# Performance work log

Measured on AMD Instinct MI355X. Metric: run time of the kernel, lower is better.

The kernel has to match this reference:

```python
import jax, jax.numpy as jnp
import numpy as np

B, M, F_IN, DX, K, L, N_ALL = 8192, 10, 128, 128, 64, 32, 100000
NN = M - 1          # n_neigh
INF = float(M)


def layer_norm(x, g, b, eps=1e-5):
    mu = x.mean(-1, keepdims=True)
    var = ((x - mu) ** 2).mean(-1, keepdims=True)
    return (x - mu) * jax.lax.rsqrt(var + eps) * g + b


def bfs_dists(adj, mask):
    # normalized all-pairs hop distances via repeated boolean matmul (m=10 fixed)
    adj_bin = (adj > 1e-5).astype(jnp.float32)
    eye = jnp.eye(M, dtype=bool)
    d = jnp.where(eye[None], 0.0, jnp.where(adj_bin > 0, 1.0, INF))
    curr = adj_bin
    for k in range(2, M):
        curr = jnp.matmul(curr, adj_bin)
        d = jnp.where((curr > 0) & (d == INF), float(k), d)
    mask2 = mask[:, :, None] * mask[:, None, :]
    d = jnp.where(mask2 == 0, INF, d)
    return d / float(M)


def compute_sw(zb, zp, theta, vmask):
    # sliced Wasserstein-2 between batch point clouds [B,NN,d] and prototypes [K,NN,d]
    tn = theta / jnp.linalg.norm(theta, axis=1, keepdims=True)
    pb = jnp.einsum('bmd,ld->bml', zb, tn)
    pp = jnp.einsum('kmd,ld->kml', zp, tn)
    idx = jnp.argsort(pb, axis=1)
    pbs = jnp.take_along_axis(pb, idx, axis=1)
    pps = jnp.sort(pp, axis=1)
    w = jnp.take_along_axis(jnp.broadcast_to(vmask[:, :, None], pb.shape), idx, axis=1)
    w = w / (w.sum(axis=1, keepdims=True) + 1e-9)
    # sum_m w*(pb-pp)^2 expanded to avoid materializing [B,K,NN,L]
    t1 = (w * pbs ** 2).sum(axis=1)                   # [B,L]
    t2 = jnp.einsum('bml,kml->bkl', w * pbs, pps)     # [B,K,L]
    t3 = jnp.einsum('bml,kml->bkl', w, pps ** 2)
    return (t1[:, None, :] - 2.0 * t2 + t3).mean(axis=-1)


def compute_radial(rb, rp, vmask):
    idx = jnp.argsort(rb, axis=1)
    rbs = jnp.take_along_axis(rb, idx, axis=1)
    rps = jnp.sort(rp, axis=1)
    w = jnp.take_along_axis(vmask, idx, axis=1)
    w = w / (w.sum(axis=1, keepdims=True) + 1e-9)
    return (((rbs[:, None, :] - rps[None]) ** 2) * w[:, None, :]).sum(-1)


def setup_inputs() -> dict:
    key = jax.random.key(0)
    ks = jax.random.split(key, 16)
    up = (jax.random.uniform(ks[0], (B, M, M)) < 0.3).astype(jnp.float32)
    adj = jnp.maximum(up, up.transpose(0, 2, 1)) * (1.0 - jnp.eye(M))
    features = jax.random.normal(ks[1], (N_ALL, F_IN), jnp.float32)
    idxs = jax.random.randint(ks[2], (B, M), 0, N_ALL + 1)   # N_ALL == padding index
    rn = lambda k, s, sc=0.02: sc * jax.random.normal(k, s, jnp.float32)
    params = dict(
        x_lin_w=rn(ks[3], (F_IN, DX), 0.05), x_lin_b=jnp.zeros((DX,)),
        x_ln_g=jnp.ones((DX,)), x_ln_b=jnp.zeros((DX,)),
        s_ln_g=jnp.ones((NN,)), s_ln_b=jnp.zeros((NN,)),
        theta_x=jax.random.normal(ks[4], (L, DX), jnp.float32),
        theta_s=jax.random.normal(ks[5], (L, NN), jnp.float32),
        alpha_raw=jnp.zeros(()),
        an_w1=rn(ks[6], (DX, 32), 0.1), an_b1=jnp.zeros((32,)),
        an_w2=rn(ks[7], (32, 1), 0.1), an_b2=jnp.zeros((1,)),
        wn_w1=rn(ks[8], (2 * DX, 32), 0.1), wn_b1=jnp.zeros((32,)),
        wn_w2=rn(ks[9], (32, 1), 0.1), wn_b2=jnp.zeros((1,)),
        w_raw=jnp.zeros(()),
        proto_root=jax.random.normal(ks[10], (K, F_IN), jnp.float32),
        proto_neigh=jax.random.normal(ks[11], (K, NN, F_IN), jnp.float32),
        proto_rad=jax.random.uniform(ks[12], (K, NN)),
        proto_dn=jax.random.uniform(ks[13], (NN * (NN - 1) // 2, K), minval=-0.5, maxval=0.5),
        log_gamma=jnp.asarray(np.log(0.01), jnp.float32),
    )
    return {"adj": adj, "features": features, "idxs": idxs, **params}


def reference(adj, features, idxs, x_lin_w, x_lin_b, x_ln_g, x_ln_b, s_ln_g, s_ln_b,
              theta_x, theta_s, alpha_raw, an_w1, an_b1, an_w2, an_b2,
              wn_w1, wn_b1, wn_w2, wn_b2, w_raw,
              proto_root, proto_neigh, proto_rad, proto_dn, log_gamma):
    b = adj.shape[0]
    x_all = jnp.concatenate([features, jnp.zeros((1, F_IN), features.dtype)], 0)
    x_patch = x_all[idxs]                             # [B,M,F]
    x_root, x_neigh = x_patch[:, 0], x_patch[:, 1:]
    vmask = (idxs[:, 1:] != N_ALL).astype(jnp.float32)   # [B,NN]
    lin = lambda x: x @ x_lin_w + x_lin_b
    h_root = layer_norm(lin(x_root), x_ln_g, x_ln_b)
    h_proto_root = layer_norm(lin(proto_root), x_ln_g, x_ln_b)
    d_root_feat = (jnp.sum(h_root ** 2, -1)[:, None] + jnp.sum(h_proto_root ** 2, -1)[None]
                   - 2.0 * h_root @ h_proto_root.T)   # squared cdist [B,K]
    full_mask = jnp.concatenate([jnp.ones((b, 1), jnp.float32), vmask], 1)
    dists_full = bfs_dists(adj, full_mask)
    d_radial_str = compute_radial(dists_full[:, 0, 1:], proto_rad, vmask)
    h_neigh = layer_norm(lin(x_neigh), x_ln_g, x_ln_b)     # dropout = identity (eval)
    h_proto_neigh = layer_norm(lin(proto_neigh), x_ln_g, x_ln_b)
    sw_neigh_feat = compute_sw(h_neigh, h_proto_neigh, theta_x, vmask)
    hs_neigh = layer_norm(jnp.sort(dists_full[:, 1:, 1:], axis=1), s_ln_g, s_ln_b)
    ti, tj = np.triu_indices(NN, 1)
    C = jnp.zeros((K, NN, NN)).at[:, ti, tj].set(jax.nn.sigmoid(proto_dn).T)
    C = C + C.transpose(0, 2, 1)
    hs_proto = layer_norm(jnp.sort(C, axis=1), s_ln_g, s_ln_b)
    sw_neigh_str = compute_sw(hs_neigh, hs_proto, theta_s, vmask)
    h_pooled = (h_neigh * vmask[:, :, None]).sum(1) / (vmask.sum(1, keepdims=True) + 1e-9)
    alpha_logit = jnp.maximum(h_pooled @ an_w1 + an_b1, 0.0) @ an_w2 + an_b2   # [B,1]
    alpha = jax.nn.sigmoid(alpha_raw + alpha_logit)
    # pairwise w_net([h_root; h_proto_root]) without materializing [B,K,2*DX]
    hb = h_root @ wn_w1[:DX] + wn_b1                   # [B,32]
    hp = h_proto_root @ wn_w1[DX:]                     # [K,32]
    w_logit = (jnp.maximum(hb[:, None] + hp[None], 0.0) @ wn_w2)[..., 0] + wn_b2[0]
    w = jax.nn.sigmoid(w_raw + w_logit)                # [B,K]
    d_feat = w * d_root_feat + (1.0 - w) * sw_neigh_feat
    d_str = w * d_radial_str + (1.0 - w) * sw_neigh_str
    d_fgw = alpha * d_feat + (1.0 - alpha) * d_str
    return jnp.exp(-jnp.exp(log_gamma) * d_fgw)        # [B,K]
```

## Files before the change

### kernel.cpp

```cpp
#include <hip/hip_runtime.h>
#include <hip/hip_bf16.h>

typedef unsigned short u16;
typedef __attribute__((ext_vector_type(8))) short short8;
typedef __attribute__((ext_vector_type(4))) float f32x4;

#define NN 9
#define DX 128
#define KP 64
#define LL 32
#define NALL 100000
#define BMAX 8192
#define NBM 16
#define NBP 64

#define MFMA(a, b, c) __builtin_amdgcn_mfma_f32_16x16x32_bf16(a, b, c, 0, 0, 0)
#define WFENCE() __threadfence_block()

__device__ __align__(16) float g_tns[LL * NN];
__device__ __align__(16) float g_hprn[KP];
__device__ __align__(16) float g_hpt[32 * KP];
__device__ __align__(16) float g_rpst[NN * KP];
__device__ __align__(16) u16   g_hx[BMAX * 10 * DX];
__device__ __align__(16) u16   g_pW[16384];
__device__ __align__(16) u16   g_pBt[4096];
__device__ __align__(16) u16   g_pBr[8192];
__device__ __align__(16) u16   g_pBx[36864];
__device__ __align__(16) u16   g_pBs[36864];
__device__ __align__(16) u16   g_pAn[4096];
__device__ __align__(16) u16   g_pWn[4096];

__device__ __forceinline__ float bf2f(u16 u) {
    union { unsigned u; float f; } v; v.u = ((unsigned)u) << 16; return v.f;
}
__device__ __forceinline__ u16 f2bf(float f) {
    __hip_bfloat16 h = __float2bfloat16(f);
    union { __hip_bfloat16 h; u16 u; } v; v.h = h; return v.u;
}
__device__ __forceinline__ float ldv(const void* p, long i, int f32) {
    return f32 ? ((const float*)p)[i] : bf2f(((const u16*)p)[i]);
}
__device__ __forceinline__ float sigmoidf(float x) { return 1.f / (1.f + expf(-x)); }

__device__ __forceinline__ int bfrag_idx(int ksteps, int ncol, int kd) {
    int ntile = ncol >> 4, n = ncol & 15;
    int kstep = kd >> 5, quad = (kd >> 3) & 3, j = kd & 7;
    return ((ntile * ksteps + kstep) * 64 + quad * 16 + n) * 8 + j;
}

__device__ __forceinline__ void rank9(const float* v, int* r) {
#pragma unroll
    for (int m = 0; m < 9; m++) {
        int rk = 0;
#pragma unroll
        for (int n = 0; n < 9; n++)
            rk += (v[n] < v[m]) || (v[n] == v[m] && n < m);
        r[m] = rk;
    }
}

__global__ __launch_bounds__(256) void k_pack(
    const void* xlw, const void* theta_x, const void* theta_s,
    const void* an_w1, const void* wn_w1, const void* xlg) {
    int t = threadIdx.x;
    const int f32 = (((const u16*)xlg)[0] == 0);
    if (blockIdx.x == 0) {
        for (int i = t; i < 16384; i += 256) {
            int c = i >> 7, d = i & 127;
            g_pW[bfrag_idx(4, d, c)] = f2bf(ldv(xlw, i, f32));
        }
    } else if (blockIdx.x == 1) {
        if (t < 32) {
            float s = 0;
            for (int d = 0; d < 128; d++) { float v = ldv(theta_x, t * 128 + d, f32); s = fmaf(v, v, s); }
            float inv = 1.f / sqrtf(s);
            for (int d = 0; d < 128; d++)
                g_pBt[bfrag_idx(4, t, d)] = f2bf(ldv(theta_x, t * 128 + d, f32) * inv);
        } else if (t < 64) {
            int l = t - 32;
            float s = 0;
            for (int j = 0; j < 9; j++) { float v = ldv(theta_s, l * 9 + j, f32); s = fmaf(v, v, s); }
            float inv = 1.f / sqrtf(s);
            for (int j = 0; j < 9; j++) g_tns[l * 9 + j] = ldv(theta_s, l * 9 + j, f32) * inv;
        }
    } else {
        for (int i = t; i < 4096; i += 256) {
            int d = i >> 5, j = i & 31;
            g_pAn[bfrag_idx(4, j, d)] = f2bf(ldv(an_w1, i, f32));
            g_pWn[bfrag_idx(4, j, d)] = f2bf(ldv(wn_w1, i, f32));
        }
    }
}

__global__ __launch_bounds__(256, 4) void k_lin(
    const void* feat, const int* idxs,
    const void* proto_root, const void* proto_neigh,
    const void* xlb, const void* xlg, const void* xlbt,
    const void* slg, const void* slb, const void* wn_w1,
    const void* proto_rad, const void* proto_dn, int B) {
    __shared__ __align__(16) u16   WfL[16384];
    __shared__ __align__(16) u16   hXpb[1280];
    __shared__ __align__(16) float pbX[288];
    __shared__ __align__(16) float Cm[84];
    __shared__ __align__(16) float hsnP[84];

    int t = threadIdx.x, lane = t & 63, w = t >> 6;
    const int f32 = (((const u16*)xlg)[0] == 0);
    int fm = lane & 15, quad = lane >> 4;
    bool isProto = (blockIdx.x < (unsigned)NBP);
    int rcap = isProto ? 10 : 60;
    int base = isProto ? blockIdx.x * 10 : (blockIdx.x - NBP) * 60;
    int rowT = isProto ? KP * 10 : B * 10;

    {
        const short8* src = (const short8*)g_pW;
        short8* dst = (short8*)WfL;
#pragma unroll
        for (int i = 0; i < 8; i++) dst[t + 256 * i] = src[t + 256 * i];
    }

    int lr = w * 16 + fm, gr = base + lr;
    bool azero = true;
    const void* abuf = feat; long aoff = 0;
    if (lr < rcap && gr < rowT) {
        if (!isProto) {
            int id = idxs[gr];
            if (id != NALL) { azero = false; aoff = (long)id * 128; }
        } else {
            int rr = gr % 10; azero = false;
            if (rr < 9) { abuf = proto_neigh; aoff = (long)((gr / 10) * 9 + rr) * 128; }
            else        { abuf = proto_root;  aoff = (long)(gr / 10) * 128; }
        }
    }
    short8 af[4];
#pragma unroll
    for (int ks = 0; ks < 4; ks++) af[ks] = (short8){0, 0, 0, 0, 0, 0, 0, 0};
    if (!azero) {
        if (f32) {
#pragma unroll
            for (int ks = 0; ks < 4; ks++) {
                const f32x4* src = (const f32x4*)((const float*)abuf + aoff + ks * 32 + quad * 8);
                f32x4 v0 = src[0], v1 = src[1];
                u16* ap = (u16*)&af[ks];
#pragma unroll
                for (int j = 0; j < 4; j++) { ap[j] = f2bf(v0[j]); ap[4 + j] = f2bf(v1[j]); }
            }
        } else {
#pragma unroll
            for (int ks = 0; ks < 4; ks++)
                af[ks] = *(const short8*)((const u16*)abuf + aoff + ks * 32 + quad * 8);
        }
    }
    float bias8[8], gg8[8], bb8[8];
#pragma unroll
    for (int nt = 0; nt < 8; nt++) {
        int col = nt * 16 + fm;
        bias8[nt] = ldv(xlb, col, f32);
        gg8[nt]   = ldv(xlg, col, f32);
        bb8[nt]   = ldv(xlbt, col, f32);
    }
    __syncthreads();

    if (w * 16 < rcap) {
        f32x4 acc[8];
#pragma unroll
        for (int nt = 0; nt < 8; nt++) acc[nt] = (f32x4){0.f, 0.f, 0.f, 0.f};
#pragma unroll
        for (int ks = 0; ks < 4; ks++) {
#pragma unroll
            for (int nt = 0; nt < 8; nt++) {
                short8 bf = *(const short8*)(WfL + ((nt * 4 + ks) * 64 + lane) * 8);
                acc[nt] = MFMA(af[ks], bf, acc[nt]);
            }
        }
#pragma unroll
        for (int reg = 0; reg < 4; reg++) {
            float s = 0, q = 0;
#pragma unroll
            for (int nt = 0; nt < 8; nt++) {
                float v = acc[nt][reg] + bias8[nt];
                s += v; q = fmaf(v, v, q);
            }
#pragma unroll
            for (int m = 1; m < 16; m <<= 1) { s += __shfl_xor(s, m); q += __shfl_xor(q, m); }
            float mu = s * (1.f / 128.f);
            float var = fmaxf(q * (1.f / 128.f) - mu * mu, 0.f);
            float rs = rsqrtf(var + 1e-5f);
            int rowD = w * 16 + quad * 4 + reg, grD = base + rowD;
            if (rowD < rcap && grD < rowT) {
#pragma unroll
                for (int nt = 0; nt < 8; nt++) {
                    float val = (acc[nt][reg] + bias8[nt] - mu) * rs * gg8[nt] + bb8[nt];
                    if (!isProto) g_hx[grD * 128 + nt * 16 + fm] = f2bf(val);
                    else          hXpb[rowD * 128 + nt * 16 + fm] = f2bf(val);
                }
            }
        }
    }
    if (!isProto) return;

    __syncthreads();
    int kb = blockIdx.x;

    for (int i = t; i < 128; i += 256)
        g_pBr[bfrag_idx(4, kb, i)] = hXpb[1152 + i];
    if (w == 0) {
        float v0 = bf2f(hXpb[1152 + lane]);
        float v1 = bf2f(hXpb[1216 + lane]);
        float q = v0 * v0 + v1 * v1;
#pragma unroll
        for (int m = 32; m >= 1; m >>= 1) q += __shfl_xor(q, m);
        if (lane == 0) g_hprn[kb] = q;
    }
    {
        int j = t >> 3, sub = t & 7;
        float a = 0;
#pragma unroll
        for (int dd = 0; dd < 16; dd++) {
            int d = sub * 16 + dd;
            a = fmaf(bf2f(hXpb[1152 + d]), ldv(wn_w1, (128 + d) * 32 + j, f32), a);
        }
        a += __shfl_xor(a, 1);
        a += __shfl_xor(a, 2);
        a += __shfl_xor(a, 4);
        if (sub == 0) g_hpt[j * 64 + kb] = a;
    }
    if (t == 0) {
        float v[9]; int r[9];
#pragma unroll
        for (int m = 0; m < 9; m++) v[m] = ldv(proto_rad, kb * 9 + m, f32);
        rank9(v, r);
#pragma unroll
        for (int m = 0; m < 9; m++) g_rpst[r[m] * 64 + kb] = v[m];
    }
    if (w == 0) {
        f32x4 acc0 = {0.f, 0.f, 0.f, 0.f}, acc1 = {0.f, 0.f, 0.f, 0.f};
        const u16* arow = hXpb + fm * 128;
#pragma unroll
        for (int ks = 0; ks < 4; ks++) {
            short8 afp = {0, 0, 0, 0, 0, 0, 0, 0};
            if (fm < 9) afp = *(const short8*)(arow + ks * 32 + quad * 8);
            short8 b0 = *(const short8*)(g_pBt + ((0 * 4 + ks) * 64 + lane) * 8);
            short8 b1 = *(const short8*)(g_pBt + ((1 * 4 + ks) * 64 + lane) * 8);
            acc0 = MFMA(afp, b0, acc0);
            acc1 = MFMA(afp, b1, acc1);
        }
#pragma unroll
        for (int reg = 0; reg < 4; reg++) {
            int row = quad * 4 + reg;
            if (row < 9) {
                pbX[row * 32 + fm]      = acc0[reg];
                pbX[row * 32 + 16 + fm] = acc1[reg];
            }
        }
    }
    for (int i = t; i < 81; i += 256) {
        int ii = i / 9, jj = i % 9; float v = 0.f;
        if (ii != jj) {
            int a = (ii < jj) ? ii : jj, b2 = (ii < jj) ? jj : ii;
            int p = a * 8 - a * (a - 1) / 2 + (b2 - a - 1);
            v = sigmoidf(ldv(proto_dn, p * 64 + kb, f32));
        }
        Cm[i] = v;
    }
    __syncthreads();
    if (t < 32) {
        float v[9]; int r[9];
#pragma unroll
        for (int m = 0; m < 9; m++) v[m] = pbX[m * 32 + t];
        rank9(v, r);
#pragma unroll
        for (int m = 0; m < 9; m++) {
            int kd = t * 9 + r[m];
            g_pBx[bfrag_idx(18, kb, kd)]       = f2bf(v[m] * v[m]);
            g_pBx[bfrag_idx(18, kb, 288 + kd)] = f2bf(v[m]);
        }
    }
    if (t >= 64 && t < 73) {
        int col = t - 64;
        float v[9]; int r[9];
#pragma unroll
        for (int j = 0; j < 9; j++) v[j] = Cm[j * 9 + col];
        rank9(v, r);
#pragma unroll
        for (int j = 0; j < 9; j++) Cm[r[j] * 9 + col] = v[j];
    }
    __syncthreads();
    if (t < 9) {
        float mu = 0;
#pragma unroll
        for (int j = 0; j < 9; j++) mu += Cm[t * 9 + j];
        mu *= (1.f / 9.f);
        float var = 0;
#pragma unroll
        for (int j = 0; j < 9; j++) { float d0 = Cm[t * 9 + j] - mu; var = fmaf(d0, d0, var); }
        var *= (1.f / 9.f);
        float rs = rsqrtf(var + 1e-5f);
#pragma unroll
        for (int j = 0; j < 9; j++)
            hsnP[t * 9 + j] = (Cm[t * 9 + j] - mu) * rs * ldv(slg, j, f32) + ldv(slb, j, f32);
    }
    __syncthreads();
    if (t < 32) {
#pragma unroll
        for (int m = 0; m < 9; m++) {
            float a = 0;
#pragma unroll
            for (int j = 0; j < 9; j++) a = fmaf(hsnP[m * 9 + j], g_tns[t * 9 + j], a);
            pbX[m * 32 + t] = a;
        }
    }
    __syncthreads();
    if (t < 32) {
        float v[9]; int r[9];
#pragma unroll
        for (int m = 0; m < 9; m++) v[m] = pbX[m * 32 + t];
        rank9(v, r);
#pragma unroll
        for (int m = 0; m < 9; m++) {
            int kd = t * 9 + r[m];
            g_pBs[bfrag_idx(18, kb, kd)]       = f2bf(v[m] * v[m]);
            g_pBs[bfrag_idx(18, kb, 288 + kd)] = f2bf(v[m]);
        }
    }
}

struct M3 {
    u16   Cf[NBM][584];
    u16   Cs[NBM][584];
    u16   hpoolb[NBM][136];
    float pb[NBM][288];
    float df[NBM][100];
    float hst[NBM][81];
    float drad[NBM][65];
    float hbv[NBM][33];
    float rbss[NBM][9], wrad[NBM][9];
    float sc[NBM][9];
};
__global__ __launch_bounds__(1024, 8) void k_main(
    const void* adj, const int* idxs,
    const void* slg, const void* slb,
    const void* an_b1, const void* an_w2, const void* an_b2,
    const void* wn_b1, const void* wn_w2, const void* wn_b2,
    const void* alpha_raw, const void* w_raw, const void* log_gamma,
    const void* xlg, void* out, int B) {
    __shared__ __align__(16) M3 S;
    int t = threadIdx.x, lane = t & 63, w = t >> 6;
    const int f32 = (((const u16*)xlg)[0] == 0);
    int fm = lane & 15, quad = lane >> 4;
    int bw = blockIdx.x * NBM + w;
    bool bv = (bw < B);

    unsigned long long mb = 0; float nv = 1e-9f, inv = 0.f;

    if (bv) {
        bool valid = false;
        if (lane < 10) {
            int id = idxs[bw * 10 + lane];
            valid = (lane == 0) || (id != NALL);
        }
        mb = __ballot(valid);
        nv = (float)__popcll(mb & 0x3FEull) + 1e-9f;
        inv = 1.f / nv;
        unsigned rowbits = 0;
        if (lane < 10) {
            for (int j = 0; j < 10; j++)
                if (ldv(adj, (long)bw * 100 + lane * 10 + j, f32) > 1e-5f) rowbits |= 1u << j;
        }
        int dl[10];
#pragma unroll
        for (int j = 0; j < 10; j++) dl[j] = (j == lane) ? 0 : (((rowbits >> j) & 1) ? 1 : 10);
        unsigned reach = (lane < 10) ? (rowbits | (1u << lane)) : 0u;
        for (int s = 2; s <= 9; s++) {
            unsigned nr = reach;
#pragma unroll
            for (int j = 0; j < 10; j++) {
                unsigned rj = __shfl(rowbits, j);
                if ((reach >> j) & 1) nr |= rj;
            }
            unsigned add = nr & ~reach;
#pragma unroll
            for (int j = 0; j < 10; j++) if ((add >> j) & 1) dl[j] = s;
            reach = nr;
            if (__all(add == 0)) break;
        }
        if (lane < 10) {
            int mi = (int)((mb >> lane) & 1);
#pragma unroll
            for (int j = 0; j < 10; j++) {
                int mj = (int)((mb >> j) & 1);
                S.df[w][lane * 10 + j] = (mi && mj) ? (float)dl[j] * 0.1f : 1.0f;
            }
        }
        {
            float v[9];
#pragma unroll
            for (int m = 0; m < 9; m++) {
                float vm = ((mb >> (1 + m)) & 1) ? (float)dl[1 + m] * 0.1f : 1.0f;
                v[m] = __shfl(vm, 0);
            }
            if (lane < 9) {
                float mine = v[0];
#pragma unroll
                for (int m = 1; m < 9; m++) if (lane == m) mine = v[m];
                int rk = 0;
#pragma unroll
                for (int n = 0; n < 9; n++) rk += (v[n] < mine) || (v[n] == mine && n < lane);
                S.rbss[w][rk] = mine;
                S.wrad[w][rk] = (((mb >> (1 + lane)) & 1) ? 1.f : 0.f) * inv;
            }
        }
        {
            u16 u0 = g_hx[bw * 1280 + lane], u1 = g_hx[bw * 1280 + 64 + lane];
            float v0 = bf2f(u0), v1 = bf2f(u1);
            float q = v0 * v0 + v1 * v1;
#pragma unroll
            for (int m = 32; m >= 1; m >>= 1) q += __shfl_xor(q, m);
            if (lane == 0) S.sc[w][1] = q;
        }
        for (int dd = lane; dd < 128; dd += 64) {
            float a = 0;
#pragma unroll
            for (int m = 0; m < 9; m++) {
                float hv = bf2f(g_hx[bw * 1280 + (1 + m) * 128 + dd]);
                float msk = ((mb >> (1 + m)) & 1) ? 1.f : 0.f;
                a = fmaf(hv, msk, a);
            }
            S.hpoolb[w][dd] = f2bf(a * inv);
        }
        {
            f32x4 acc0 = {0.f, 0.f, 0.f, 0.f}, acc1 = {0.f, 0.f, 0.f, 0.f};
            const u16* arow = g_hx + (bw * 10 + 1 + fm) * 128;
#pragma unroll
            for (int ks = 0; ks < 4; ks++) {
                short8 af = {0, 0, 0, 0, 0, 0, 0, 0};
                if (fm < 9) af = *(const short8*)(arow + ks * 32 + quad * 8);
                short8 b0 = *(const short8*)(g_pBt + ((0 * 4 + ks) * 64 + lane) * 8);
                short8 b1 = *(const short8*)(g_pBt + ((1 * 4 + ks) * 64 + lane) * 8);
                acc0 = MFMA(af, b0, acc0);
                acc1 = MFMA(af, b1, acc1);
            }
#pragma unroll
            for (int reg = 0; reg < 4; reg++) {
                int row = quad * 4 + reg;
                if (row < 9) {
                    S.pb[w][row * 32 + fm]      = acc0[reg];
                    S.pb[w][row * 32 + 16 + fm] = acc1[reg];
                }
            }
        }
        WFENCE();

        {
            float t1 = 0;
            if (lane < 32) {
                float v[9]; int r[9];
#pragma unroll
                for (int m = 0; m < 9; m++) v[m] = S.pb[w][m * 32 + lane];
                rank9(v, r);
#pragma unroll
                for (int m = 0; m < 9; m++) {
                    float wgt = (((mb >> (1 + m)) & 1) ? 1.f : 0.f) * inv;
                    int slot = lane * 9 + r[m];
                    S.Cf[w][slot]       = f2bf(wgt);
                    S.Cf[w][288 + slot] = f2bf(-2.f * wgt * v[m]);
                    t1 = fmaf(wgt * v[m], v[m], t1);
                }
            }
#pragma unroll
            for (int m = 16; m >= 1; m >>= 1) t1 += __shfl_xor(t1, m);
            if (lane == 0) S.sc[w][3] = t1;
        }
        if (lane < 9) {
            float v[9]; int r[9];
#pragma unroll
            for (int i = 0; i < 9; i++) v[i] = S.df[w][(1 + i) * 10 + 1 + lane];
            rank9(v, r);
#pragma unroll
            for (int i = 0; i < 9; i++) S.hst[w][r[i] * 9 + lane] = v[i];
        }
        {
            float acc = 0;
#pragma unroll
            for (int m = 0; m < 9; m++) {
                float d0 = S.rbss[w][m] - g_rpst[m * 64 + lane];
                acc = fmaf(d0 * d0, S.wrad[w][m], acc);
            }
            S.drad[w][lane] = acc;
        }
        WFENCE();

        if (lane < 9) {
            float vv[9];
#pragma unroll
            for (int j = 0; j < 9; j++) vv[j] = S.hst[w][lane * 9 + j];
            float mu = 0;
#pragma unroll
            for (int j = 0; j < 9; j++) mu += vv[j];
            mu *= (1.f / 9.f);
            float var = 0;
#pragma unroll
            for (int j = 0; j < 9; j++) { float d0 = vv[j] - mu; var = fmaf(d0, d0, var); }
            var *= (1.f / 9.f);
            float rs = rsqrtf(var + 1e-5f);
#pragma unroll
            for (int j = 0; j < 9; j++)
                S.hst[w][lane * 9 + j] = (vv[j] - mu) * rs * ldv(slg, j, f32) + ldv(slb, j, f32);
        }
        WFENCE();

        {
            int l = lane & 31;
            int m0 = (lane < 32) ? 0 : 5, m1 = (lane < 32) ? 5 : 9;
            for (int m = m0; m < m1; m++) {
                float a = 0;
#pragma unroll
                for (int j = 0; j < 9; j++) a = fmaf(S.hst[w][m * 9 + j], g_tns[l * 9 + j], a);
                S.pb[w][m * 32 + l] = a;
            }
        }
        WFENCE();

        {
            float t1 = 0;
            if (lane < 32) {
                float v[9]; int r[9];
#pragma unroll
                for (int m = 0; m < 9; m++) v[m] = S.pb[w][m * 32 + lane];
                rank9(v, r);
#pragma unroll
                for (int m = 0; m < 9; m++) {
                    float wgt = (((mb >> (1 + m)) & 1) ? 1.f : 0.f) * inv;
                    int slot = lane * 9 + r[m];
                    S.Cs[w][slot]       = f2bf(wgt);
                    S.Cs[w][288 + slot] = f2bf(-2.f * wgt * v[m]);
                    t1 = fmaf(wgt * v[m], v[m], t1);
                }
            }
#pragma unroll
            for (int m = 16; m >= 1; m >>= 1) t1 += __shfl_xor(t1, m);
            if (lane == 0) S.sc[w][4] = t1;
        }
    }
    __syncthreads();

    f32x4 rd = {0.f, 0.f, 0.f, 0.f};
    f32x4 accF = {0.f, 0.f, 0.f, 0.f}, accS = {0.f, 0.f, 0.f, 0.f};
    if (w < 4) {
#pragma unroll
        for (int ks = 0; ks < 4; ks++) {
            short8 af = {0, 0, 0, 0, 0, 0, 0, 0};
            int bb = blockIdx.x * NBM + fm;
            if (bb < B) af = *(const short8*)(g_hx + (long)bb * 1280 + ks * 32 + quad * 8);
            short8 bfr = *(const short8*)(g_pBr + ((w * 4 + ks) * 64 + lane) * 8);
            rd = MFMA(af, bfr, rd);
        }
#pragma unroll
        for (int ks = 0; ks < 18; ks++) {
            short8 aF = *(const short8*)(S.Cf[fm] + ks * 32 + quad * 8);
            short8 aS = *(const short8*)(S.Cs[fm] + ks * 32 + quad * 8);
            short8 bF = *(const short8*)(g_pBx + ((w * 18 + ks) * 64 + lane) * 8);
            short8 bS = *(const short8*)(g_pBs + ((w * 18 + ks) * 64 + lane) * 8);
            accF = MFMA(aF, bF, accF);
            accS = MFMA(aS, bS, accS);
        }
    } else if (w == 4) {
        f32x4 a0 = {0.f, 0.f, 0.f, 0.f}, a1 = {0.f, 0.f, 0.f, 0.f};
#pragma unroll
        for (int ks = 0; ks < 4; ks++) {
            short8 af = {0, 0, 0, 0, 0, 0, 0, 0};
            int bb = blockIdx.x * NBM + fm;
            if (bb < B) af = *(const short8*)(g_hx + (long)bb * 1280 + ks * 32 + quad * 8);
            short8 b0 = *(const short8*)(g_pWn + ((0 * 4 + ks) * 64 + lane) * 8);
            short8 b1 = *(const short8*)(g_pWn + ((1 * 4 + ks) * 64 + lane) * 8);
            a0 = MFMA(af, b0, a0);
            a1 = MFMA(af, b1, a1);
        }
        float wb0 = ldv(wn_b1, fm, f32), wb1 = ldv(wn_b1, 16 + fm, f32);
#pragma unroll
        for (int reg = 0; reg < 4; reg++) {
            int b = quad * 4 + reg;
            S.hbv[b][fm]      = a0[reg] + wb0;
            S.hbv[b][16 + fm] = a1[reg] + wb1;
        }
    } else if (w == 5) {
        f32x4 a0 = {0.f, 0.f, 0.f, 0.f}, a1 = {0.f, 0.f, 0.f, 0.f};
#pragma unroll
        for (int ks = 0; ks < 4; ks++) {
            short8 af = *(const short8*)(S.hpoolb[fm] + ks * 32 + quad * 8);
            short8 b0 = *(const short8*)(g_pAn + ((0 * 4 + ks) * 64 + lane) * 8);
            short8 b1 = *(const short8*)(g_pAn + ((1 * 4 + ks) * 64 + lane) * 8);
            a0 = MFMA(af, b0, a0);
            a1 = MFMA(af, b1, a1);
        }
        float ab0 = ldv(an_b1, fm, f32), ab1 = ldv(an_b1, 16 + fm, f32);
        float aw0 = ldv(an_w2, fm, f32), aw1 = ldv(an_w2, 16 + fm, f32);
        float araw = ldv(alpha_raw, 0, f32), ab2 = ldv(an_b2, 0, f32);
#pragma unroll
        for (int reg = 0; reg < 4; reg++) {
            float s = fmaxf(a0[reg] + ab0, 0.f) * aw0 + fmaxf(a1[reg] + ab1, 0.f) * aw1;
            s += __shfl_xor(s, 1); s += __shfl_xor(s, 2);
            s += __shfl_xor(s, 4); s += __shfl_xor(s, 8);
            if (fm == 0) S.sc[quad * 4 + reg][2] = sigmoidf(araw + s + ab2);
        }
    }
    __syncthreads();

    if (w < 4) {
        int k = w * 16 + fm;
        float wb2 = ldv(wn_b2, 0, f32);
        float wr  = ldv(w_raw, 0, f32);
        float gamma = expf(ldv(log_gamma, 0, f32));
        float hprnk = g_hprn[k];
        float wl[4] = {0.f, 0.f, 0.f, 0.f};
#pragma unroll 4
        for (int j = 0; j < 32; j++) {
            float hptv = g_hpt[j * 64 + k];
            float w2v = ldv(wn_w2, j, f32);
#pragma unroll
            for (int reg = 0; reg < 4; reg++)
                wl[reg] = fmaf(fmaxf(S.hbv[quad * 4 + reg][j] + hptv, 0.f), w2v, wl[reg]);
        }
#pragma unroll
        for (int reg = 0; reg < 4; reg++) {
            int b = quad * 4 + reg, bb = blockIdx.x * NBM + b;
            if (bb >= B) continue;
            float swf = (S.sc[b][3] + accF[reg]) * (1.f / 32.f);
            float sws = (S.sc[b][4] + accS[reg]) * (1.f / 32.f);
            float drfk = S.sc[b][1] + hprnk - 2.f * rd[reg];
            float wgt = sigmoidf(wr + wl[reg] + wb2);
            float dfeat = wgt * drfk + (1.f - wgt) * swf;
            float dstr  = wgt * S.drad[b][k] + (1.f - wgt) * sws;
            float al = S.sc[b][2];
            float dfgw = al * dfeat + (1.f - al) * dstr;
            if (!(dfgw == dfgw)) dfgw = 1e30f;
            float res = expf(-gamma * dfgw);
            if (f32) ((float*)out)[(long)bb * 64 + k] = res;
            else     ((u16*)out)[(long)bb * 64 + k] = f2bf(res);
        }
    }
}

extern "C" void kernel_launch(void* const* d_in, const int* in_sizes, int n_in,
                              void* d_out, int out_size, void* d_ws, size_t ws_size,
                              hipStream_t stream) {
    const void* adj  = d_in[0];
    const void* feat = d_in[1];
    const int*  idxs = (const int*)d_in[2];
    const void* xlw  = d_in[3];
    const void* xlb  = d_in[4];
    const void* xlg  = d_in[5];
    const void* xlbt = d_in[6];
    const void* slg  = d_in[7];
    const void* slb  = d_in[8];
    const void* thx  = d_in[9];
    const void* ths  = d_in[10];
    const void* araw = d_in[11];
    const void* anw1 = d_in[12];
    const void* anb1 = d_in[13];
    const void* anw2 = d_in[14];
    const void* anb2 = d_in[15];
    const void* wnw1 = d_in[16];
    const void* wnb1 = d_in[17];
    const void* wnw2 = d_in[18];
    const void* wnb2 = d_in[19];
    const void* wraw = d_in[20];
    const void* prt  = d_in[21];
    const void* prn  = d_in[22];
    const void* prad = d_in[23];
    const void* pdn  = d_in[24];
    const void* lgam = d_in[25];
    int B = in_sizes[2] / 10;
    int NBQ = (B * 10 + 59) / 60;

    k_pack<<<3, 256, 0, stream>>>(xlw, thx, ths, anw1, wnw1, xlg);
    k_lin<<<NBP + NBQ, 256, 0, stream>>>(feat, idxs, prt, prn,
                                         xlb, xlg, xlbt, slg, slb, wnw1,
                                         prad, pdn, B);
    k_main<<<(B + NBM - 1) / NBM, 1024, 0, stream>>>(adj, idxs, slg, slb,
                                  anb1, anw2, anb2, wnb1, wnw2, wnb2,
                                  araw, wraw, lgam, xlg, d_out, B);
}
```

Baseline: 208.9 us.

## Fuse batch feature linear+layernorm into main kernel, keep hidden rows in LDS

Moves the per-batch gather, linear projection and layer norm of node features from the separate k_lin kernel into k_main. Each wave computes its own 10x128 hidden rows with MFMA and stores them in a padded shared-memory tile, so the global g_hx buffer is no longer written and then read back. k_lin becomes a small prototype-only kernel. The cost is more shared memory per block (launch bounds drop from 8 to 4 blocks per SM) and weight fragments now read from global per wave instead of from LDS.

```diff
diff --git a/kernel.cpp b/kernel.cpp
--- a/kernel.cpp
+++ b/kernel.cpp
@@ -10,9 +10,9 @@
 #define KP 64
 #define LL 32
 #define NALL 100000
-#define BMAX 8192
 #define NBM 16
-#define NBP 64
+#define HXR 136
+#define HXB (10 * HXR)
 
 #define MFMA(a, b, c) __builtin_amdgcn_mfma_f32_16x16x32_bf16(a, b, c, 0, 0, 0)
 #define WFENCE() __threadfence_block()
@@ -21,7 +21,6 @@
 __device__ __align__(16) float g_hprn[KP];
 __device__ __align__(16) float g_hpt[32 * KP];
 __device__ __align__(16) float g_rpst[NN * KP];
-__device__ __align__(16) u16   g_hx[BMAX * 10 * DX];
 __device__ __align__(16) u16   g_pW[16384];
 __device__ __align__(16) u16   g_pBt[4096];
 __device__ __align__(16) u16   g_pBr[8192];
@@ -92,12 +91,11 @@
     }
 }
 
-__global__ __launch_bounds__(256, 4) void k_lin(
-    const void* feat, const int* idxs,
+__global__ __launch_bounds__(256, 4) void k_proto(
     const void* proto_root, const void* proto_neigh,
     const void* xlb, const void* xlg, const void* xlbt,
     const void* slg, const void* slb, const void* wn_w1,
-    const void* proto_rad, const void* proto_dn, int B) {
+    const void* proto_rad, const void* proto_dn) {
     __shared__ __align__(16) u16   WfL[16384];
     __shared__ __align__(16) u16   hXpb[1280];
     __shared__ __align__(16) float pbX[288];
@@ -107,10 +105,7 @@
     int t = threadIdx.x, lane = t & 63, w = t >> 6;
     const int f32 = (((const u16*)xlg)[0] == 0);
     int fm = lane & 15, quad = lane >> 4;
-    bool isProto = (blockIdx.x < (unsigned)NBP);
-    int rcap = isProto ? 10 : 60;
-    int base = isProto ? blockIdx.x * 10 : (blockIdx.x - NBP) * 60;
-    int rowT = isProto ? KP * 10 : B * 10;
+    int kb = blockIdx.x;
 
     {
         const short8* src = (const short8*)g_pW;
@@ -119,23 +114,17 @@
         for (int i = 0; i < 8; i++) dst[t + 256 * i] = src[t + 256 * i];
     }
 
-    int lr = w * 16 + fm, gr = base + lr;
-    bool azero = true;
-    const void* abuf = feat; long aoff = 0;
-    if (lr < rcap && gr < rowT) {
-        if (!isProto) {
-            int id = idxs[gr];
-            if (id != NALL) { azero = false; aoff = (long)id * 128; }
-        } else {
-            int rr = gr % 10; azero = false;
-            if (rr < 9) { abuf = proto_neigh; aoff = (long)((gr / 10) * 9 + rr) * 128; }
-            else        { abuf = proto_root;  aoff = (long)(gr / 10) * 128; }
-        }
+    int lr = w * 16 + fm;
+    const void* abuf = proto_root; long aoff = 0;
+    bool arow = (lr < 10);
+    if (arow) {
+        if (lr < 9) { abuf = proto_neigh; aoff = (long)(kb * 9 + lr) * 128; }
+        else        { abuf = proto_root;  aoff = (long)kb * 128; }
     }
     short8 af[4];
 #pragma unroll
     for (int ks = 0; ks < 4; ks++) af[ks] = (short8){0, 0, 0, 0, 0, 0, 0, 0};
-    if (!azero) {
+    if (arow) {
         if (f32) {
 #pragma unroll
             for (int ks = 0; ks < 4; ks++) {
@@ -161,7 +150,7 @@
     }
     __syncthreads();
 
-    if (w * 16 < rcap) {
+    if (w == 0) {
         f32x4 acc[8];
 #pragma unroll
         for (int nt = 0; nt < 8; nt++) acc[nt] = (f32x4){0.f, 0.f, 0.f, 0.f};
@@ -186,21 +175,17 @@
             float mu = s * (1.f / 128.f);
             float var = fmaxf(q * (1.f / 128.f) - mu * mu, 0.f);
             float rs = rsqrtf(var + 1e-5f);
-            int rowD = w * 16 + quad * 4 + reg, grD = base + rowD;
-            if (rowD < rcap && grD < rowT) {
+            int rowD = quad * 4 + reg;
+            if (rowD < 10) {
 #pragma unroll
                 for (int nt = 0; nt < 8; nt++) {
                     float val = (acc[nt][reg] + bias8[nt] - mu) * rs * gg8[nt] + bb8[nt];
-                    if (!isProto) g_hx[grD * 128 + nt * 16 + fm] = f2bf(val);
-                    else          hXpb[rowD * 128 + nt * 16 + fm] = f2bf(val);
+                    hXpb[rowD * 128 + nt * 16 + fm] = f2bf(val);
                 }
             }
         }
     }
-    if (!isProto) return;
-
     __syncthreads();
-    int kb = blockIdx.x;
 
     for (int i = t; i < 128; i += 256)
         g_pBr[bfrag_idx(4, kb, i)] = hXpb[1152 + i];
@@ -235,11 +220,11 @@
     }
     if (w == 0) {
         f32x4 acc0 = {0.f, 0.f, 0.f, 0.f}, acc1 = {0.f, 0.f, 0.f, 0.f};
-        const u16* arow = hXpb + fm * 128;
+        const u16* arow2 = hXpb + fm * 128;
 #pragma unroll
         for (int ks = 0; ks < 4; ks++) {
             short8 afp = {0, 0, 0, 0, 0, 0, 0, 0};
-            if (fm < 9) afp = *(const short8*)(arow + ks * 32 + quad * 8);
+            if (fm < 9) afp = *(const short8*)(arow2 + ks * 32 + quad * 8);
             short8 b0 = *(const short8*)(g_pBt + ((0 * 4 + ks) * 64 + lane) * 8);
             short8 b1 = *(const short8*)(g_pBt + ((1 * 4 + ks) * 64 + lane) * 8);
             acc0 = MFMA(afp, b0, acc0);
@@ -329,6 +314,7 @@
     u16   Cf[NBM][584];
     u16   Cs[NBM][584];
     u16   hpoolb[NBM][136];
+    u16   hX[NBM][HXB];
     float pb[NBM][288];
     float df[NBM][100];
     float hst[NBM][81];
@@ -337,13 +323,14 @@
     float rbss[NBM][9], wrad[NBM][9];
     float sc[NBM][9];
 };
-__global__ __launch_bounds__(1024, 8) void k_main(
-    const void* adj, const int* idxs,
+__global__ __launch_bounds__(1024, 4) void k_main(
+    const void* adj, const void* feat, const int* idxs,
     const void* slg, const void* slb,
+    const void* xlb, const void* xlg, const void* xlbt,
     const void* an_b1, const void* an_w2, const void* an_b2,
     const void* wn_b1, const void* wn_w2, const void* wn_b2,
     const void* alpha_raw, const void* w_raw, const void* log_gamma,
-    const void* xlg, void* out, int B) {
+    void* out, int B) {
     __shared__ __align__(16) M3 S;
     int t = threadIdx.x, lane = t & 63, w = t >> 6;
     const int f32 = (((const u16*)xlg)[0] == 0);
@@ -354,6 +341,31 @@
     unsigned long long mb = 0; float nv = 1e-9f, inv = 0.f;
 
     if (bv) {
+        bool azero = true; long aoff = 0;
+        if (fm < 10) {
+            int id = idxs[bw * 10 + fm];
+            if (id != NALL) { azero = false; aoff = (long)id * 128; }
+        }
+        short8 af[4];
+#pragma unroll
+        for (int ks = 0; ks < 4; ks++) af[ks] = (short8){0, 0, 0, 0, 0, 0, 0, 0};
+        if (!azero) {
+            if (f32) {
+#pragma unroll
+                for (int ks = 0; ks < 4; ks++) {
+                    const f32x4* src = (const f32x4*)((const float*)feat + aoff + ks * 32 + quad * 8);
+                    f32x4 v0 = src[0], v1 = src[1];
+                    u16* ap = (u16*)&af[ks];
+#pragma unroll
+                    for (int j = 0; j < 4; j++) { ap[j] = f2bf(v0[j]); ap[4 + j] = f2bf(v1[j]); }
+                }
+            } else {
+#pragma unroll
+                for (int ks = 0; ks < 4; ks++)
+                    af[ks] = *(const short8*)((const u16*)feat + aoff + ks * 32 + quad * 8);
+            }
+        }
+
         bool valid = false;
         if (lane < 10) {
             int id = idxs[bw * 10 + lane];
@@ -410,9 +422,54 @@
                 S.wrad[w][rk] = (((mb >> (1 + lane)) & 1) ? 1.f : 0.f) * inv;
             }
         }
+
         {
-            u16 u0 = g_hx[bw * 1280 + lane], u1 = g_hx[bw * 1280 + 64 + lane];
-            float v0 = bf2f(u0), v1 = bf2f(u1);
+            float bias8[8], gg8[8], bb8[8];
+#pragma unroll
+            for (int nt = 0; nt < 8; nt++) {
+                int col = nt * 16 + fm;
+                bias8[nt] = ldv(xlb, col, f32);
+                gg8[nt]   = ldv(xlg, col, f32);
+                bb8[nt]   = ldv(xlbt, col, f32);
+            }
+            f32x4 acc[8];
+#pragma unroll
+            for (int nt = 0; nt < 8; nt++) acc[nt] = (f32x4){0.f, 0.f, 0.f, 0.f};
+#pragma unroll
+            for (int ks = 0; ks < 4; ks++) {
+#pragma unroll
+                for (int nt = 0; nt < 8; nt++) {
+                    short8 bf = *(const short8*)(g_pW + ((nt * 4 + ks) * 64 + lane) * 8);
+                    acc[nt] = MFMA(af[ks], bf, acc[nt]);
+                }
+            }
+#pragma unroll
+            for (int reg = 0; reg < 4; reg++) {
+                float s = 0, q = 0;
+#pragma unroll
+                for (int nt = 0; nt < 8; nt++) {
+                    float v = acc[nt][reg] + bias8[nt];
+                    s += v; q = fmaf(v, v, q);
+                }
+#pragma unroll
+                for (int m = 1; m < 16; m <<= 1) { s += __shfl_xor(s, m); q += __shfl_xor(q, m); }
+                float mu = s * (1.f / 128.f);
+                float var = fmaxf(q * (1.f / 128.f) - mu * mu, 0.f);
+                float rs = rsqrtf(var + 1e-5f);
+                int rowD = quad * 4 + reg;
+                if (rowD < 10) {
+#pragma unroll
+                    for (int nt = 0; nt < 8; nt++) {
+                        float val = (acc[nt][reg] + bias8[nt] - mu) * rs * gg8[nt] + bb8[nt];
+                        S.hX[w][rowD * HXR + nt * 16 + fm] = f2bf(val);
+                    }
+                }
+            }
+        }
+        WFENCE();
+
+        {
+            float v0 = bf2f(S.hX[w][lane]), v1 = bf2f(S.hX[w][64 + lane]);
             float q = v0 * v0 + v1 * v1;
 #pragma unroll
             for (int m = 32; m >= 1; m >>= 1) q += __shfl_xor(q, m);
@@ -422,7 +479,7 @@
             float a = 0;
 #pragma unroll
             for (int m = 0; m < 9; m++) {
-                float hv = bf2f(g_hx[bw * 1280 + (1 + m) * 128 + dd]);
+                float hv = bf2f(S.hX[w][(1 + m) * HXR + dd]);
                 float msk = ((mb >> (1 + m)) & 1) ? 1.f : 0.f;
                 a = fmaf(hv, msk, a);
             }
@@ -430,15 +487,15 @@
         }
         {
             f32x4 acc0 = {0.f, 0.f, 0.f, 0.f}, acc1 = {0.f, 0.f, 0.f, 0.f};
-            const u16* arow = g_hx + (bw * 10 + 1 + fm) * 128;
+            const u16* arow = S.hX[w] + (1 + fm) * HXR;
 #pragma unroll
             for (int ks = 0; ks < 4; ks++) {
-                short8 af = {0, 0, 0, 0, 0, 0, 0, 0};
-                if (fm < 9) af = *(const short8*)(arow + ks * 32 + quad * 8);
+                short8 afn = {0, 0, 0, 0, 0, 0, 0, 0};
+                if (fm < 9) afn = *(const short8*)(arow + ks * 32 + quad * 8);
                 short8 b0 = *(const short8*)(g_pBt + ((0 * 4 + ks) * 64 + lane) * 8);
                 short8 b1 = *(const short8*)(g_pBt + ((1 * 4 + ks) * 64 + lane) * 8);
-                acc0 = MFMA(af, b0, acc0);
-                acc1 = MFMA(af, b1, acc1);
+                acc0 = MFMA(afn, b0, acc0);
+                acc1 = MFMA(afn, b1, acc1);
             }
 #pragma unroll
             for (int reg = 0; reg < 4; reg++) {
@@ -550,8 +607,8 @@
 #pragma unroll
         for (int ks = 0; ks < 4; ks++) {
             short8 af = {0, 0, 0, 0, 0, 0, 0, 0};
-            int bb = blockIdx.x * NBM + fm;
-            if (bb < B) af = *(const short8*)(g_hx + (long)bb * 1280 + ks * 32 + quad * 8);
+            if (blockIdx.x * NBM + fm < B)
+                af = *(const short8*)(S.hX[fm] + ks * 32 + quad * 8);
             short8 bfr = *(const short8*)(g_pBr + ((w * 4 + ks) * 64 + lane) * 8);
             rd = MFMA(af, bfr, rd);
         }
@@ -569,8 +626,8 @@
 #pragma unroll
         for (int ks = 0; ks < 4; ks++) {
             short8 af = {0, 0, 0, 0, 0, 0, 0, 0};
-            int bb = blockIdx.x * NBM + fm;
-            if (bb < B) af = *(const short8*)(g_hx + (long)bb * 1280 + ks * 32 + quad * 8);
+            if (blockIdx.x * NBM + fm < B)
+                af = *(const short8*)(S.hX[fm] + ks * 32 + quad * 8);
             short8 b0 = *(const short8*)(g_pWn + ((0 * 4 + ks) * 64 + lane) * 8);
             short8 b1 = *(const short8*)(g_pWn + ((1 * 4 + ks) * 64 + lane) * 8);
             a0 = MFMA(af, b0, a0);
@@ -671,13 +728,12 @@
     const void* pdn  = d_in[24];
     const void* lgam = d_in[25];
     int B = in_sizes[2] / 10;
-    int NBQ = (B * 10 + 59) / 60;
 
     k_pack<<<3, 256, 0, stream>>>(xlw, thx, ths, anw1, wnw1, xlg);
-    k_lin<<<NBP + NBQ, 256, 0, stream>>>(feat, idxs, prt, prn,
-                                         xlb, xlg, xlbt, slg, slb, wnw1,
-                                         prad, pdn, B);
-    k_main<<<(B + NBM - 1) / NBM, 1024, 0, stream>>>(adj, idxs, slg, slb,
+    k_proto<<<KP, 256, 0, stream>>>(prt, prn, xlb, xlg, xlbt, slg, slb, wnw1,
+                                    prad, pdn);
+    k_main<<<(B + NBM - 1) / NBM, 1024, 0, stream>>>(adj, feat, idxs, slg, slb,
+                                  xlb, xlg, xlbt,
                                   anb1, anw2, anb2, wnb1, wnw2, wnb2,
-                                  araw, wraw, lgam, xlg, d_out, B);
-}
+                                  araw, wraw, lgam, d_out, B);
+}
```

Result: slower. 226.8 us (+8.6%).

## Compute masked neighbor pooling and root norm in linear kernel epilogue

Applied to the files above, without the earlier changes.

The linear+layernorm kernel now stages its output tile in shared memory (reusing the weight buffer) and copies it to global memory with coalesced 16-byte stores. It also computes, per batch item, the masked mean of the neighbor embeddings and the squared norm of the root embedding, and writes both to new global buffers. The downstream kernel reads these precomputed values instead of re-reading ten rows of g_hx and reducing them per warp. This adds an extra block barrier and an extra epilogue pass in k_lin, in exchange for less global traffic and less reduction work in the consumer.

```diff
diff --git a/kernel.cpp b/kernel.cpp
--- a/kernel.cpp
+++ b/kernel.cpp
@@ -22,6 +22,8 @@
 __device__ __align__(16) float g_hpt[32 * KP];
 __device__ __align__(16) float g_rpst[NN * KP];
 __device__ __align__(16) u16   g_hx[BMAX * 10 * DX];
+__device__ __align__(16) u16   g_hpool[BMAX * DX];
+__device__ __align__(16) float g_hrn[BMAX];
 __device__ __align__(16) u16   g_pW[16384];
 __device__ __align__(16) u16   g_pBt[4096];
 __device__ __align__(16) u16   g_pBr[8192];
@@ -103,6 +105,7 @@
     __shared__ __align__(16) float pbX[288];
     __shared__ __align__(16) float Cm[84];
     __shared__ __align__(16) float hsnP[84];
+    u16* hS = WfL;
 
     int t = threadIdx.x, lane = t & 63, w = t >> 6;
     const int f32 = (((const u16*)xlg)[0] == 0);
@@ -161,10 +164,10 @@
     }
     __syncthreads();
 
+    f32x4 acc[8];
+#pragma unroll
+    for (int nt = 0; nt < 8; nt++) acc[nt] = (f32x4){0.f, 0.f, 0.f, 0.f};
     if (w * 16 < rcap) {
-        f32x4 acc[8];
-#pragma unroll
-        for (int nt = 0; nt < 8; nt++) acc[nt] = (f32x4){0.f, 0.f, 0.f, 0.f};
 #pragma unroll
         for (int ks = 0; ks < 4; ks++) {
 #pragma unroll
@@ -173,6 +176,10 @@
                 acc[nt] = MFMA(af[ks], bf, acc[nt]);
             }
         }
+    }
+    __syncthreads();
+
+    if (w * 16 < rcap) {
 #pragma unroll
         for (int reg = 0; reg < 4; reg++) {
             float s = 0, q = 0;
@@ -191,15 +198,60 @@
 #pragma unroll
                 for (int nt = 0; nt < 8; nt++) {
                     float val = (acc[nt][reg] + bias8[nt] - mu) * rs * gg8[nt] + bb8[nt];
-                    if (!isProto) g_hx[grD * 128 + nt * 16 + fm] = f2bf(val);
+                    if (!isProto) hS[rowD * 128 + nt * 16 + fm] = f2bf(val);
                     else          hXpb[rowD * 128 + nt * 16 + fm] = f2bf(val);
                 }
             }
         }
     }
-    if (!isProto) return;
-
-    __syncthreads();
+    __syncthreads();
+
+    if (!isProto) {
+        int nrows = rowT - base; if (nrows > 60) nrows = 60;
+        {
+            const short8* src = (const short8*)hS;
+            short8* dst = (short8*)(g_hx + (long)base * 128);
+            for (int i = t; i < nrows * 16; i += 256) dst[i] = src[i];
+        }
+        if (t < 192) {
+            int b = t >> 5, l = t & 31;
+            int bg = base / 10 + b;
+            if (b * 10 < nrows && bg < B) {
+                unsigned msk9 = 0; int cnt = 0;
+#pragma unroll
+                for (int m = 0; m < 9; m++) {
+                    if (idxs[bg * 10 + 1 + m] != NALL) { msk9 |= 1u << m; cnt++; }
+                }
+                float invb = 1.f / ((float)cnt + 1e-9f);
+                float rq = 0;
+                unsigned r01, r23;
+                {
+                    u16 o[4];
+#pragma unroll
+                    for (int cc = 0; cc < 4; cc++) {
+                        int c = l * 4 + cc;
+                        float a = 0;
+#pragma unroll
+                        for (int m = 0; m < 9; m++)
+                            if ((msk9 >> m) & 1) a += bf2f(hS[(b * 10 + 1 + m) * 128 + c]);
+                        o[cc] = f2bf(a * invb);
+                        float rv = bf2f(hS[(b * 10) * 128 + c]);
+                        rq = fmaf(rv, rv, rq);
+                    }
+                    r01 = (unsigned)o[0] | ((unsigned)o[1] << 16);
+                    r23 = (unsigned)o[2] | ((unsigned)o[3] << 16);
+                }
+                unsigned* gp = (unsigned*)(g_hpool + (long)bg * 128);
+                gp[l * 2]     = r01;
+                gp[l * 2 + 1] = r23;
+#pragma unroll
+                for (int m = 16; m >= 1; m >>= 1) rq += __shfl_xor(rq, m);
+                if (l == 0) g_hrn[bg] = rq;
+            }
+        }
+        return;
+    }
+
     int kb = blockIdx.x;
 
     for (int i = t; i < 128; i += 256)
@@ -235,11 +287,11 @@
     }
     if (w == 0) {
         f32x4 acc0 = {0.f, 0.f, 0.f, 0.f}, acc1 = {0.f, 0.f, 0.f, 0.f};
-        const u16* arow = hXpb + fm * 128;
+        const u16* arow2 = hXpb + fm * 128;
 #pragma unroll
         for (int ks = 0; ks < 4; ks++) {
             short8 afp = {0, 0, 0, 0, 0, 0, 0, 0};
-            if (fm < 9) afp = *(const short8*)(arow + ks * 32 + quad * 8);
+            if (fm < 9) afp = *(const short8*)(arow2 + ks * 32 + quad * 8);
             short8 b0 = *(const short8*)(g_pBt + ((0 * 4 + ks) * 64 + lane) * 8);
             short8 b1 = *(const short8*)(g_pBt + ((1 * 4 + ks) * 64 + lane) * 8);
             acc0 = MFMA(afp, b0, acc0);
@@ -410,24 +462,8 @@
                 S.wrad[w][rk] = (((mb >> (1 + lane)) & 1) ? 1.f : 0.f) * inv;
             }
         }
-        {
-            u16 u0 = g_hx[bw * 1280 + lane], u1 = g_hx[bw * 1280 + 64 + lane];
-            float v0 = bf2f(u0), v1 = bf2f(u1);
-            float q = v0 * v0 + v1 * v1;
-#pragma unroll
-            for (int m = 32; m >= 1; m >>= 1) q += __shfl_xor(q, m);
-            if (lane == 0) S.sc[w][1] = q;
-        }
-        for (int dd = lane; dd < 128; dd += 64) {
-            float a = 0;
-#pragma unroll
-            for (int m = 0; m < 9; m++) {
-                float hv = bf2f(g_hx[bw * 1280 + (1 + m) * 128 + dd]);
-                float msk = ((mb >> (1 + m)) & 1) ? 1.f : 0.f;
-                a = fmaf(hv, msk, a);
-            }
-            S.hpoolb[w][dd] = f2bf(a * inv);
-        }
+        if (lane == 0) S.sc[w][1] = g_hrn[bw];
+        ((unsigned*)S.hpoolb[w])[lane] = ((const unsigned*)(g_hpool + (long)bw * 128))[lane];
         {
             f32x4 acc0 = {0.f, 0.f, 0.f, 0.f}, acc1 = {0.f, 0.f, 0.f, 0.f};
             const u16* arow = g_hx + (bw * 10 + 1 + fm) * 128;
```

After: 211.8 us. No clear change (+1.4%).
